# Performance work log

Hardware: AMD Instinct MI355X
Metric: run time of the kernel (lower is better)

The kernel has to match this reference:

```python
import jax, jax.numpy as jnp
import numpy as np

NUM_RAYS = 8192
NUM_POINTS = 1024
NEAR, FAR = 0.1, 6.0


def setup_inputs() -> dict:
    key = jax.random.key(0)
    k_rgb, k_alpha, k_jit, k_dir = jax.random.split(key, 4)
    raw_rgb_per_point = jax.random.uniform(k_rgb, (NUM_RAYS, NUM_POINTS, 3), dtype=jnp.float32)
    raw_alpha = jax.random.normal(k_alpha, (NUM_RAYS, NUM_POINTS), dtype=jnp.float32)
    # Monotonically increasing z values per ray (linspace + stratified jitter)
    t = jnp.linspace(0.0, 1.0, NUM_POINTS)[None, :]  # [1, P]
    jitter = jax.random.uniform(k_jit, (NUM_RAYS, NUM_POINTS), dtype=jnp.float32) / NUM_POINTS
    z_vals = (NEAR + (FAR - NEAR) * jnp.clip(t + jitter, 0.0, 1.0)).astype(jnp.float32)
    z_vals = jnp.sort(z_vals, axis=-1)
    rays_dir = jax.random.normal(k_dir, (NUM_RAYS, 3), dtype=jnp.float32)
    pruning_mask = jnp.ones((NUM_RAYS, NUM_POINTS), dtype=bool)
    return {
        "raw_rgb_per_point": raw_rgb_per_point,
        "raw_alpha": raw_alpha,
        "z_vals": z_vals,
        "rays_dir": rays_dir,
        "pruning_mask": pruning_mask,
        "points_per_ray": NUM_POINTS,
    }


def reference(raw_rgb_per_point, raw_alpha, z_vals, rays_dir, pruning_mask, points_per_ray):
    # Faithful eval-mode (is_training=False) translation of Renderer._compose_rays.
    corrective_factor = float(points_per_ray) / 1024.0
    FAR_DIST = 1e10

    # Distances between adjacent samples, last one padded to "infinity".
    dists = z_vals[..., 1:] - z_vals[..., :-1]                      # [R, P-1]
    dists = jnp.concatenate(
        [dists, jnp.full_like(dists[..., :1], FAR_DIST)], axis=-1)  # [R, P]
    dists = dists * jnp.linalg.norm(rays_dir, axis=-1, keepdims=True)

    # raw2alpha: 1 - exp(-relu(raw) * dist * cf)
    alpha = 1.0 - jnp.exp(-jax.nn.relu(raw_alpha) * dists * corrective_factor)  # [R, P]

    # Exclusive cumulative transmittance, then weights.
    trans = jnp.cumprod(
        jnp.concatenate([jnp.ones_like(alpha[:, :1]), 1.0 - alpha + 1e-10], axis=-1),
        axis=-1)[:, :-1]                                            # [R, P]
    weights = alpha * trans                                         # [R, P]

    rgb = jnp.einsum("rp,rpc->rc", weights, raw_rgb_per_point)      # [R, 3]
    accumulated_weights = jnp.sum(weights, axis=-1)                 # [R]

    depth = (jnp.sum(weights[:, :-1] * z_vals[:, :-1], axis=-1)
             + (1.0 - accumulated_weights + weights[:, -1]) * z_vals[:, -1])  # [R]

    disparity = 1.0 / jnp.maximum(1e-4, depth / accumulated_weights)          # [R]

    return rgb, accumulated_weights, depth, disparity
```

## Files before the change

kernel.cpp:

```cpp
#include <hip/hip_runtime.h>


#define NUM_RAYS 8192
#define P 1024
#define BLOCK 256

__global__ __launch_bounds__(256) void compose_rays_kernel(
    const float* __restrict__ rgb_in,
    const float* __restrict__ raw_alpha,
    const float* __restrict__ z_vals,
    const float* __restrict__ rays_dir,
    const int*   __restrict__ ppr,
    float* __restrict__ out)
{
    const int r    = blockIdx.x;
    const int t    = threadIdx.x;
    const int lane = t & 63;
    const int wid  = t >> 6;

    const float cf = (float)(*ppr) * (1.0f / 1024.0f);

    const float dx = rays_dir[r * 3 + 0];
    const float dy = rays_dir[r * 3 + 1];
    const float dz = rays_dir[r * 3 + 2];
    const float nrm = sqrtf(dx * dx + dy * dy + dz * dz);

    const size_t rowP = (size_t)r * P;
    const float4 a4 = *(const float4*)(raw_alpha + rowP + 4 * t);
    const float4 z4 = *(const float4*)(z_vals    + rowP + 4 * t);
    float z_next = 0.0f;
    if (t < BLOCK - 1) z_next = z_vals[rowP + 4 * t + 4];

    float av[4] = {a4.x, a4.y, a4.z, a4.w};
    float zv[4] = {z4.x, z4.y, z4.z, z4.w};
    float dists[4];
    dists[0] = (z4.y - z4.x) * nrm;
    dists[1] = (z4.z - z4.y) * nrm;
    dists[2] = (z4.w - z4.z) * nrm;
    dists[3] = ((t == BLOCK - 1) ? 1e10f : (z_next - z4.w)) * nrm;

    float alpha[4], om[4];
    float local_prod = 1.0f;
#pragma unroll
    for (int j = 0; j < 4; ++j) {
        float ra = fmaxf(av[j], 0.0f);
        alpha[j] = 1.0f - expf(-ra * dists[j] * cf);
        om[j]    = 1.0f - alpha[j] + 1e-10f;
        local_prod *= om[j];
    }

    float v = local_prod;
#pragma unroll
    for (int off = 1; off < 64; off <<= 1) {
        float n = __shfl_up(v, off);
        if (lane >= off) v *= n;
    }

    __shared__ float wave_tot[4];
    __shared__ float red[4][5];
    __shared__ float last_wz[2];
    if (lane == 63) wave_tot[wid] = v;
    __syncthreads();

    float excl = __shfl_up(v, 1);
    if (lane == 0) excl = 1.0f;
#pragma unroll
    for (int w = 0; w < 3; ++w)
        if (wid > w) excl *= wave_tot[w];

    const float* rgbp = rgb_in + (size_t)r * (P * 3) + 12 * t;
    const float4 c0 = *(const float4*)(rgbp + 0);
    const float4 c1 = *(const float4*)(rgbp + 4);
    const float4 c2 = *(const float4*)(rgbp + 8);
    float rgbv[12] = {c0.x, c0.y, c0.z, c0.w, c1.x, c1.y, c1.z, c1.w,
                      c2.x, c2.y, c2.z, c2.w};

    float trun = excl;
    float ws = 0.f, rs = 0.f, gs = 0.f, bs = 0.f, ds = 0.f;
#pragma unroll
    for (int j = 0; j < 4; ++j) {
        float w = alpha[j] * trun;
        ws += w;
        rs += w * rgbv[3 * j + 0];
        gs += w * rgbv[3 * j + 1];
        bs += w * rgbv[3 * j + 2];
        if (4 * t + j < P - 1) {
            ds += w * zv[j];
        } else {
            last_wz[0] = w;
            last_wz[1] = zv[j];
        }
        trun *= om[j];
    }

#pragma unroll
    for (int off = 32; off > 0; off >>= 1) {
        ws += __shfl_down(ws, off);
        rs += __shfl_down(rs, off);
        gs += __shfl_down(gs, off);
        bs += __shfl_down(bs, off);
        ds += __shfl_down(ds, off);
    }
    if (lane == 0) {
        red[wid][0] = ws; red[wid][1] = rs; red[wid][2] = gs;
        red[wid][3] = bs; red[wid][4] = ds;
    }
    __syncthreads();

    if (t == 0) {
        float W = 0.f, R_ = 0.f, G = 0.f, B = 0.f, D = 0.f;
#pragma unroll
        for (int w = 0; w < 4; ++w) {
            W  += red[w][0];
            R_ += red[w][1];
            G  += red[w][2];
            B  += red[w][3];
            D  += red[w][4];
        }
        const float wl = last_wz[0];
        const float zl = last_wz[1];
        const float depth = D + (1.0f - W + wl) * zl;
        const float disp  = 1.0f / fmaxf(1e-4f, depth / W);
        out[r * 3 + 0] = R_;
        out[r * 3 + 1] = G;
        out[r * 3 + 2] = B;
        out[3 * NUM_RAYS + r] = W;
        out[4 * NUM_RAYS + r] = depth;
        out[5 * NUM_RAYS + r] = disp;
    }
}

extern "C" void kernel_launch(void* const* d_in, const int* in_sizes, int n_in,
                              void* d_out, int out_size, void* d_ws, size_t ws_size,
                              hipStream_t stream) {
    const float* rgb_in    = (const float*)d_in[0];
    const float* raw_alpha = (const float*)d_in[1];
    const float* z_vals    = (const float*)d_in[2];
    const float* rays_dir  = (const float*)d_in[3];
    const int*   ppr       = (const int*)d_in[5];
    float* out = (float*)d_out;

    compose_rays_kernel<<<NUM_RAYS, BLOCK, 0, stream>>>(
        rgb_in, raw_alpha, z_vals, rays_dir, ppr, out);
}
```

Measured before the change: 30.66 us.

## Map one wavefront per ray and drop block-level shared-memory synchronisation

Each 64-lane wavefront now handles a whole ray by looping over four 256-point chunks, carrying the transmittance product between chunks. Four rays share a block. This removes the shared-memory cross-wave scan, both __syncthreads calls and the final serial reduction by thread 0. In exchange each wave runs a longer serial chain of four scans, and fewer blocks are launched, which may leave less latency hiding for this memory-bound kernel.

```diff
diff --git a/kernel.cpp b/kernel.cpp
--- a/kernel.cpp
+++ b/kernel.cpp
@@ -4,6 +4,7 @@
 #define NUM_RAYS 8192
 #define P 1024
 #define BLOCK 256
+#define RAYS_PER_BLOCK 4
 
 __global__ __launch_bounds__(256) void compose_rays_kernel(
     const float* __restrict__ rgb_in,
@@ -13,10 +14,9 @@
     const int*   __restrict__ ppr,
     float* __restrict__ out)
 {
-    const int r    = blockIdx.x;
-    const int t    = threadIdx.x;
-    const int lane = t & 63;
-    const int wid  = t >> 6;
+    const int lane = threadIdx.x & 63;
+    const int wid  = threadIdx.x >> 6;
+    const int r    = blockIdx.x * RAYS_PER_BLOCK + wid;
 
     const float cf = (float)(*ppr) * (1.0f / 1024.0f);
 
@@ -26,72 +26,82 @@
     const float nrm = sqrtf(dx * dx + dy * dy + dz * dz);
 
     const size_t rowP = (size_t)r * P;
-    const float4 a4 = *(const float4*)(raw_alpha + rowP + 4 * t);
-    const float4 z4 = *(const float4*)(z_vals    + rowP + 4 * t);
-    float z_next = 0.0f;
-    if (t < BLOCK - 1) z_next = z_vals[rowP + 4 * t + 4];
 
-    float av[4] = {a4.x, a4.y, a4.z, a4.w};
-    float zv[4] = {z4.x, z4.y, z4.z, z4.w};
-    float dists[4];
-    dists[0] = (z4.y - z4.x) * nrm;
-    dists[1] = (z4.z - z4.y) * nrm;
-    dists[2] = (z4.w - z4.z) * nrm;
-    dists[3] = ((t == BLOCK - 1) ? 1e10f : (z_next - z4.w)) * nrm;
+    float4 z4[4];
+#pragma unroll
+    for (int it = 0; it < 4; ++it)
+        z4[it] = *(const float4*)(z_vals + rowP + it * 256 + lane * 4);
 
-    float alpha[4], om[4];
-    float local_prod = 1.0f;
+    float znext[4];
 #pragma unroll
-    for (int j = 0; j < 4; ++j) {
-        float ra = fmaxf(av[j], 0.0f);
-        alpha[j] = 1.0f - expf(-ra * dists[j] * cf);
-        om[j]    = 1.0f - alpha[j] + 1e-10f;
-        local_prod *= om[j];
+    for (int it = 0; it < 4; ++it) {
+        const float from_next_lane = __shfl_down(z4[it].x, 1);
+        const float first_of_next  = (it < 3) ? __shfl(z4[it + 1].x, 0) : 0.0f;
+        znext[it] = (lane == 63) ? first_of_next : from_next_lane;
+    }
+    const float zl = __shfl(z4[3].w, 63);
+
+    float carry = 1.0f;
+    float ws = 0.f, rs = 0.f, gs = 0.f, bs = 0.f, ds = 0.f;
+    float wlast = 0.f;
+
+#pragma unroll
+    for (int it = 0; it < 4; ++it) {
+        const float4 a4 = *(const float4*)(raw_alpha + rowP + it * 256 + lane * 4);
+        const float* rgbp = rgb_in + (size_t)r * (P * 3) + it * 768 + lane * 12;
+        const float4 c0 = *(const float4*)(rgbp + 0);
+        const float4 c1 = *(const float4*)(rgbp + 4);
+        const float4 c2 = *(const float4*)(rgbp + 8);
+
+        const float zv[4] = {z4[it].x, z4[it].y, z4[it].z, z4[it].w};
+        const float av[4] = {a4.x, a4.y, a4.z, a4.w};
+        float dists[4];
+        dists[0] = (zv[1] - zv[0]) * nrm;
+        dists[1] = (zv[2] - zv[1]) * nrm;
+        dists[2] = (zv[3] - zv[2]) * nrm;
+        dists[3] = ((it == 3 && lane == 63) ? 1e10f : (znext[it] - zv[3])) * nrm;
+
+        float alpha[4], om[4];
+        float local = 1.0f;
+#pragma unroll
+        for (int j = 0; j < 4; ++j) {
+            const float ra = fmaxf(av[j], 0.0f);
+            alpha[j] = 1.0f - expf(-ra * dists[j] * cf);
+            om[j]    = 1.0f - alpha[j] + 1e-10f;
+            local   *= om[j];
+        }
+
+        float v = local;
+#pragma unroll
+        for (int off = 1; off < 64; off <<= 1) {
+            const float n = __shfl_up(v, off);
+            if (lane >= off) v *= n;
+        }
+        const float total = __shfl(v, 63);
+        float excl = __shfl_up(v, 1);
+        if (lane == 0) excl = 1.0f;
+        excl *= carry;
+        carry *= total;
+
+        const float rgbv[12] = {c0.x, c0.y, c0.z, c0.w, c1.x, c1.y, c1.z, c1.w,
+                                c2.x, c2.y, c2.z, c2.w};
+        float trun = excl;
+#pragma unroll
+        for (int j = 0; j < 4; ++j) {
+            const float w = alpha[j] * trun;
+            ws += w;
+            rs += w * rgbv[3 * j + 0];
+            gs += w * rgbv[3 * j + 1];
+            bs += w * rgbv[3 * j + 2];
+            if (it == 3 && lane == 63 && j == 3)
+                wlast = w;
+            else
+                ds += w * zv[j];
+            trun *= om[j];
+        }
     }
 
-    float v = local_prod;
-#pragma unroll
-    for (int off = 1; off < 64; off <<= 1) {
-        float n = __shfl_up(v, off);
-        if (lane >= off) v *= n;
-    }
-
-    __shared__ float wave_tot[4];
-    __shared__ float red[4][5];
-    __shared__ float last_wz[2];
-    if (lane == 63) wave_tot[wid] = v;
-    __syncthreads();
-
-    float excl = __shfl_up(v, 1);
-    if (lane == 0) excl = 1.0f;
-#pragma unroll
-    for (int w = 0; w < 3; ++w)
-        if (wid > w) excl *= wave_tot[w];
-
-    const float* rgbp = rgb_in + (size_t)r * (P * 3) + 12 * t;
-    const float4 c0 = *(const float4*)(rgbp + 0);
-    const float4 c1 = *(const float4*)(rgbp + 4);
-    const float4 c2 = *(const float4*)(rgbp + 8);
-    float rgbv[12] = {c0.x, c0.y, c0.z, c0.w, c1.x, c1.y, c1.z, c1.w,
-                      c2.x, c2.y, c2.z, c2.w};
-
-    float trun = excl;
-    float ws = 0.f, rs = 0.f, gs = 0.f, bs = 0.f, ds = 0.f;
-#pragma unroll
-    for (int j = 0; j < 4; ++j) {
-        float w = alpha[j] * trun;
-        ws += w;
-        rs += w * rgbv[3 * j + 0];
-        gs += w * rgbv[3 * j + 1];
-        bs += w * rgbv[3 * j + 2];
-        if (4 * t + j < P - 1) {
-            ds += w * zv[j];
-        } else {
-            last_wz[0] = w;
-            last_wz[1] = zv[j];
-        }
-        trun *= om[j];
-    }
+    const float wl = __shfl(wlast, 63);
 
 #pragma unroll
     for (int off = 32; off > 0; off >>= 1) {
@@ -101,30 +111,14 @@
         bs += __shfl_down(bs, off);
         ds += __shfl_down(ds, off);
     }
+
     if (lane == 0) {
-        red[wid][0] = ws; red[wid][1] = rs; red[wid][2] = gs;
-        red[wid][3] = bs; red[wid][4] = ds;
-    }
-    __syncthreads();
-
-    if (t == 0) {
-        float W = 0.f, R_ = 0.f, G = 0.f, B = 0.f, D = 0.f;
-#pragma unroll
-        for (int w = 0; w < 4; ++w) {
-            W  += red[w][0];
-            R_ += red[w][1];
-            G  += red[w][2];
-            B  += red[w][3];
-            D  += red[w][4];
-        }
-        const float wl = last_wz[0];
-        const float zl = last_wz[1];
-        const float depth = D + (1.0f - W + wl) * zl;
-        const float disp  = 1.0f / fmaxf(1e-4f, depth / W);
-        out[r * 3 + 0] = R_;
-        out[r * 3 + 1] = G;
-        out[r * 3 + 2] = B;
-        out[3 * NUM_RAYS + r] = W;
+        const float depth = ds + (1.0f - ws + wl) * zl;
+        const float disp  = 1.0f / fmaxf(1e-4f, depth / ws);
+        out[r * 3 + 0] = rs;
+        out[r * 3 + 1] = gs;
+        out[r * 3 + 2] = bs;
+        out[3 * NUM_RAYS + r] = ws;
         out[4 * NUM_RAYS + r] = depth;
         out[5 * NUM_RAYS + r] = disp;
     }
@@ -140,6 +134,6 @@
     const int*   ppr       = (const int*)d_in[5];
     float* out = (float*)d_out;
 
-    compose_rays_kernel<<<NUM_RAYS, BLOCK, 0, stream>>>(
+    compose_rays_kernel<<<NUM_RAYS / RAYS_PER_BLOCK, BLOCK, 0, stream>>>(
         rgb_in, raw_alpha, z_vals, rays_dir, ppr, out);
 }
```

Result: no change. 31.25 us (+1.9%).
